# Performance work log

Hardware: AMD Instinct MI355X
Metric: run time of the kernel (lower is better)

Reference implementation:

```python
import jax, jax.numpy as jnp
import numpy as np

B, T, C, H = 4, 2048, 1024, 16
D = C // H


def setup_inputs() -> dict:
    key = jax.random.key(0)
    ks = jax.random.split(key, 5)
    s = C ** -0.5  # keep linear outputs O(1) like standard init
    x = jax.random.normal(ks[0], (B, T, C), dtype=jnp.float32)
    Wq = jax.random.normal(ks[1], (C, C), dtype=jnp.float32) * s
    Wk = jax.random.normal(ks[2], (C, C), dtype=jnp.float32) * s
    Wv = jax.random.normal(ks[3], (C, C), dtype=jnp.float32) * s
    Wproj = jax.random.normal(ks[4], (C, C), dtype=jnp.float32) * s
    alpha_raw = jnp.zeros((1, H, 1, 1), dtype=jnp.float32)
    beta_raw = jnp.zeros((1, H, 1, 1), dtype=jnp.float32)
    state = jnp.zeros((B, H, D, D), dtype=jnp.float32)
    return dict(x=x, Wq=Wq, Wk=Wk, Wv=Wv, Wproj=Wproj,
                alpha_raw=alpha_raw, beta_raw=beta_raw, state=state)


def reference(x, Wq, Wk, Wv, Wproj, alpha_raw, beta_raw, state):
    Bx, Tx, Cx = x.shape
    Hn = alpha_raw.shape[1]
    Dh = Cx // Hn
    # projections (torch Linear: x @ W^T), split heads -> (B, H, T, D)
    def proj(W):
        return (x @ W.T).reshape(Bx, Tx, Hn, Dh).transpose(0, 2, 1, 3)
    q, k, v = proj(Wq), proj(Wk), proj(Wv)
    # F.normalize(k, dim=-1) with eps=1e-12
    k = k / jnp.maximum(jnp.linalg.norm(k, axis=-1, keepdims=True), 1e-12)
    alpha = jax.nn.sigmoid(alpha_raw) * 0.5  # (1, H, 1, 1)
    beta = jax.nn.sigmoid(beta_raw) * 0.5

    def step(st, qkv):
        qt, kt, vt = qkv  # each (B, H, D)
        # y_t = q_t @ state^T
        y = jnp.einsum('bhe,bhde->bhd', qt, st)
        # Mk = state @ k_t
        Mk = jnp.einsum('bhde,bhe->bhd', st, kt)
        st = st - alpha * jnp.einsum('bhd,bhe->bhde', Mk, kt) \
                + beta * jnp.einsum('bhd,bhe->bhde', vt, kt)
        return st, y

    # scan over time: (T, B, H, D)
    qT = q.transpose(2, 0, 1, 3)
    kT = k.transpose(2, 0, 1, 3)
    vT = v.transpose(2, 0, 1, 3)
    state_f, ys = jax.lax.scan(step, state, (qT, kT, vT))
    y = ys.transpose(1, 0, 2, 3).reshape(Bx, Tx, Cx)  # (B, T, C)
    out = y @ Wproj.T
    return out, state_f
```

## Files before the change

kernel.cpp:

```cpp
#include <hip/hip_runtime.h>
#include <hip/hip_bf16.h>
#include <cstdint>

#define B_ 4
#define T_ 2048
#define C_ 1024
#define H_ 16
#define D_ 64
#define NC_ 32
#define L_ 64

typedef __attribute__((ext_vector_type(8))) short bf16x8;
typedef __attribute__((ext_vector_type(4))) float f32x4;

static __device__ __forceinline__ unsigned short f2bf(float f) {
  unsigned u = __float_as_uint(f);
  u += 0x7fff + ((u >> 16) & 1);
  return (unsigned short)(u >> 16);
}
static __device__ __forceinline__ float bf2f(unsigned short b) {
  return __uint_as_float(((unsigned)b) << 16);
}
static __device__ __forceinline__ int swz128(int row, int byte) {
  return row * 128 + (byte ^ ((row & 7) << 4));
}

#define LDS_BARRIER() asm volatile("s_waitcnt lgkmcnt(0)\ns_barrier" ::: "memory")

__global__ __launch_bounds__(256) void cvt_kernel(const float* __restrict__ src,
                                                  unsigned short* __restrict__ dst, int n) {
  int i = (blockIdx.x * 256 + threadIdx.x) * 4;
  if (i >= n) return;
  float4 v = *reinterpret_cast<const float4*>(src + i);
  ushort4 o;
  o.x = f2bf(v.x); o.y = f2bf(v.y); o.z = f2bf(v.z); o.w = f2bf(v.w);
  *reinterpret_cast<ushort4*>(dst + i) = o;
}

__global__ __launch_bounds__(256) void cvt_w_kernel(const float* __restrict__ wq,
                                                    const float* __restrict__ wk,
                                                    const float* __restrict__ wv,
                                                    const float* __restrict__ wp,
                                                    unsigned short* __restrict__ W3,
                                                    unsigned short* __restrict__ Wp) {
  const int g = blockIdx.x >> 10;
  const float* src = (g == 0) ? wq : (g == 1) ? wk : (g == 2) ? wv : wp;
  unsigned short* dst = (g < 3) ? (W3 + (long)g * 1048576) : Wp;
  int i = ((blockIdx.x & 1023) * 256 + threadIdx.x) * 4;
  float4 v = *reinterpret_cast<const float4*>(src + i);
  ushort4 o;
  o.x = f2bf(v.x); o.y = f2bf(v.y); o.z = f2bf(v.z); o.w = f2bf(v.w);
  *reinterpret_cast<ushort4*>(dst + i) = o;
}

template<int OUT_BF16>
__global__ __launch_bounds__(256) void gemm_bt(const unsigned short* __restrict__ A,
                                               const unsigned short* __restrict__ Bw,
                                               void* __restrict__ Cp,
                                               int M, int N, int K) {
  __shared__ __align__(16) unsigned short sA[128 * 32];
  __shared__ __align__(16) unsigned short sB[128 * 32];
  const int tid = threadIdx.x;
  const int wid = tid >> 6, lane = tid & 63;
  const int wm = wid >> 1, wn = wid & 1;
  const long blockM = (long)blockIdx.y * 128;
  const long blockN = (long)blockIdx.x * 128;

  f32x4 acc[4][4] = {};

  const int ar = lane >> 2;
  const int ac = (lane & 3) * 8;
  const unsigned short* Abase = A + (blockM + wid * 32 + ar) * (long)K + ac;
  const unsigned short* Bbase = Bw + (blockN + wid * 32 + ar) * (long)K + ac;
  char* sAb = (char*)sA + wid * 2048;
  char* sBb = (char*)sB + wid * 2048;

  for (int k0 = 0; k0 < K; k0 += 32) {
    __syncthreads();
    __builtin_amdgcn_global_load_lds((const __attribute__((address_space(1))) void*)(Abase + k0),
                                     (__attribute__((address_space(3))) void*)(sAb), 16, 0, 0);
    __builtin_amdgcn_global_load_lds((const __attribute__((address_space(1))) void*)(Abase + 16 * (long)K + k0),
                                     (__attribute__((address_space(3))) void*)(sAb + 1024), 16, 0, 0);
    __builtin_amdgcn_global_load_lds((const __attribute__((address_space(1))) void*)(Bbase + k0),
                                     (__attribute__((address_space(3))) void*)(sBb), 16, 0, 0);
    __builtin_amdgcn_global_load_lds((const __attribute__((address_space(1))) void*)(Bbase + 16 * (long)K + k0),
                                     (__attribute__((address_space(3))) void*)(sBb + 1024), 16, 0, 0);
    __syncthreads();

    const int koff = (lane >> 4) * 8;
    const int rA = wm * 64 + (lane & 15);
    const int rB = wn * 64 + (lane & 15);
    bf16x8 af[4], bfr[4];
#pragma unroll
    for (int m = 0; m < 4; ++m)
      af[m] = *reinterpret_cast<const bf16x8*>(&sA[(rA + m * 16) * 32 + koff]);
#pragma unroll
    for (int n = 0; n < 4; ++n)
      bfr[n] = *reinterpret_cast<const bf16x8*>(&sB[(rB + n * 16) * 32 + koff]);
#pragma unroll
    for (int m = 0; m < 4; ++m)
#pragma unroll
      for (int n = 0; n < 4; ++n)
        acc[m][n] = __builtin_amdgcn_mfma_f32_16x16x32_bf16(af[m], bfr[n], acc[m][n], 0, 0, 0);
  }

  const int cr = (lane >> 4) * 4;
  const int cc = lane & 15;
#pragma unroll
  for (int m = 0; m < 4; ++m) {
    long R = blockM + wm * 64 + m * 16 + cr;
#pragma unroll
    for (int n = 0; n < 4; ++n) {
      long Cc = blockN + wn * 64 + n * 16 + cc;
#pragma unroll
      for (int r = 0; r < 4; ++r) {
        if (OUT_BF16)
          ((unsigned short*)Cp)[(R + r) * (long)N + Cc] = f2bf(acc[m][n][r]);
        else
          ((float*)Cp)[(R + r) * (long)N + Cc] = acc[m][n][r];
      }
    }
  }
}

__global__ __launch_bounds__(256) void chunk_prep(
    unsigned short* __restrict__ qkv,
    const float* __restrict__ a_raw, const float* __restrict__ b_raw,
    unsigned short* __restrict__ Ubuf, unsigned short* __restrict__ Wbuf,
    unsigned short* __restrict__ SLbuf) {
  __shared__ __align__(16) unsigned short sK[64 * 64];
  __shared__ __align__(16) unsigned short sQ[64 * 64];
  __shared__ __align__(16) unsigned short sV[64 * 64];
  __shared__ float sA[64 * 64];

  const int blk = blockIdx.x;
  const int bh = blk >> 5, c = blk & 31;
  const int b = bh >> 4, h = bh & 15;
  const int tid = threadIdx.x;
  const int wid = tid >> 6, lane = tid & 63;

  const float alpha = 0.5f / (1.f + __expf(-a_raw[h]));
  const float beta  = 0.5f / (1.f + __expf(-b_raw[h]));

  {
    const int row = tid >> 2, cg = tid & 3;
    unsigned short* gp = qkv + (long)(b * 2048 + c * 64 + row) * 3072 + h * 64 + cg * 16;
    bf16x8 q0 = *(const bf16x8*)(gp);
    bf16x8 q1 = *(const bf16x8*)(gp + 8);
    bf16x8 k0 = *(const bf16x8*)(gp + 1024);
    bf16x8 k1 = *(const bf16x8*)(gp + 1024 + 8);
    bf16x8 v0 = *(const bf16x8*)(gp + 2048);
    bf16x8 v1 = *(const bf16x8*)(gp + 2048 + 8);
    float kf[16];
    float ss = 0.f;
#pragma unroll
    for (int i = 0; i < 8; ++i) { kf[i] = bf2f((unsigned short)k0[i]); ss += kf[i] * kf[i]; }
#pragma unroll
    for (int i = 0; i < 8; ++i) { kf[8 + i] = bf2f((unsigned short)k1[i]); ss += kf[8 + i] * kf[8 + i]; }
    ss += __shfl_xor(ss, 1);
    ss += __shfl_xor(ss, 2);
    const float inv = 1.f / fmaxf(sqrtf(ss), 1e-12f);
    bf16x8 n0, n1;
#pragma unroll
    for (int i = 0; i < 8; ++i) { n0[i] = (short)f2bf(kf[i] * inv); n1[i] = (short)f2bf(kf[8 + i] * inv); }
    *(bf16x8*)((char*)sK + swz128(row, cg * 32)) = n0;
    *(bf16x8*)((char*)sK + swz128(row, cg * 32 + 16)) = n1;
    *(bf16x8*)(gp + 1024) = n0;
    *(bf16x8*)(gp + 1024 + 8) = n1;
    *(bf16x8*)((char*)sQ + swz128(row, cg * 32)) = q0;
    *(bf16x8*)((char*)sQ + swz128(row, cg * 32 + 16)) = q1;
    *(bf16x8*)((char*)sV + row * 128 + cg * 32) = v0;
    *(bf16x8*)((char*)sV + row * 128 + cg * 32 + 16) = v1;
  }
  __syncthreads();

  const int rfrag = lane & 15, koff = (lane >> 4) * 8, crow = (lane >> 4) * 4;
  const int w2 = wid & 1;
  if (wid < 2) {
#pragma unroll
    for (int mt = 0; mt < 2; ++mt) {
      const int m = w2 * 2 + mt;
      const int ra = 16 * m + rfrag;
      f32x4 acc[4] = {};
#pragma unroll
      for (int ks = 0; ks < 2; ++ks) {
        bf16x8 af = *(const bf16x8*)((const char*)sK + swz128(ra, ks * 64 + koff * 2));
#pragma unroll
        for (int n = 0; n < 4; ++n) {
          bf16x8 bf = *(const bf16x8*)((const char*)sK + swz128(16 * n + rfrag, ks * 64 + koff * 2));
          acc[n] = __builtin_amdgcn_mfma_f32_16x16x32_bf16(af, bf, acc[n], 0, 0, 0);
        }
      }
#pragma unroll
      for (int n = 0; n < 4; ++n)
#pragma unroll
        for (int r = 0; r < 4; ++r)
          sA[(16 * m + crow + r) * 64 + 16 * n + rfrag] = acc[n][r];
    }
  } else {
#pragma unroll
    for (int mt = 0; mt < 2; ++mt) {
      const int m = w2 * 2 + mt;
      const int ra = 16 * m + rfrag;
      f32x4 acc[4] = {};
#pragma unroll
      for (int ks = 0; ks < 2; ++ks) {
        bf16x8 af = *(const bf16x8*)((const char*)sQ + swz128(ra, ks * 64 + koff * 2));
#pragma unroll
        for (int n = 0; n < 4; ++n) {
          bf16x8 bf = *(const bf16x8*)((const char*)sK + swz128(16 * n + rfrag, ks * 64 + koff * 2));
          acc[n] = __builtin_amdgcn_mfma_f32_16x16x32_bf16(af, bf, acc[n], 0, 0, 0);
        }
      }
#pragma unroll
      for (int n = 0; n < 4; ++n)
#pragma unroll
        for (int r = 0; r < 4; ++r) {
          int t = 16 * m + crow + r, j = 16 * n + rfrag;
          SLbuf[(long)blk * 4096 + t * 64 + j] = (j < t) ? f2bf(acc[n][r]) : (unsigned short)0;
        }
    }
  }
  __syncthreads();

  if (wid < 2) {
    const int d = lane;
    float x[64];
#pragma unroll
    for (int t = 0; t < 64; ++t) {
      float rhs;
      if (wid == 0) rhs = beta * bf2f(sV[t * 64 + d]);
      else          rhs = alpha * bf2f(*(const unsigned short*)((const char*)sK + swz128(t, 2 * d)));
      float s = 0.f;
#pragma unroll
      for (int j = 0; j < t; ++j) s = fmaf(sA[t * 64 + j], x[j], s);
      x[t] = rhs - alpha * s;
    }
    unsigned short* ob = (wid == 0 ? Ubuf : Wbuf) + (long)blk * 4096 + d;
#pragma unroll
    for (int t = 0; t < 64; ++t) ob[t * 64] = f2bf(x[t]);
  }
}

__global__ __launch_bounds__(256) void chunk_scan(
    const unsigned short* __restrict__ qkv,
    const unsigned short* __restrict__ Ubuf, const unsigned short* __restrict__ Wbuf,
    const unsigned short* __restrict__ SLbuf,
    const float* __restrict__ state_in, unsigned short* __restrict__ ybuf,
    float* __restrict__ state_out) {
  __shared__ __align__(16) unsigned short sQ[64 * 64];
  __shared__ __align__(16) unsigned short sW[64 * 64];
  __shared__ __align__(16) unsigned short sSL[64 * 64];
  __shared__ __align__(16) unsigned short sKT[64 * 64];
  __shared__ __align__(16) unsigned short sU[64 * 16];
  __shared__ __align__(16) unsigned short sGT[16 * 64];
  __shared__ __align__(16) unsigned short sS[16 * 64];

  const int blk = blockIdx.x;
  const int bh = blk >> 2, dq = blk & 3;
  const int b = bh >> 4, h = bh & 15;
  const int tid = threadIdx.x, wid = tid >> 6, lane = tid & 63;
  const int rfrag = lane & 15, koff = (lane >> 4) * 8, crow = (lane >> 4) * 4;
  const int row = tid >> 2, cg = tid & 3;

  const unsigned short* gpb = qkv + (long)(b * 2048 + row) * 3072 + h * 64 + cg * 16;
  const long tbb = ((long)(bh * 32) * 64 + row) * 64 + cg * 16;
  const long ubb = ((long)(bh * 32) * 64 + (tid >> 1)) * 64 + dq * 16 + (tid & 1) * 8;

  bf16x8 qv0, qv1, kv0, kv1, wv0, wv1, sl0, sl1, uv;
  {
    qv0 = *(const bf16x8*)gpb;
    qv1 = *(const bf16x8*)(gpb + 8);
    kv0 = *(const bf16x8*)(gpb + 1024);
    kv1 = *(const bf16x8*)(gpb + 1024 + 8);
    wv0 = *(const bf16x8*)(Wbuf + tbb);
    wv1 = *(const bf16x8*)(Wbuf + tbb + 8);
    sl0 = *(const bf16x8*)(SLbuf + tbb);
    sl1 = *(const bf16x8*)(SLbuf + tbb + 8);
    uv = (tid < 128) ? *(const bf16x8*)(Ubuf + ubb) : bf16x8{};
  }

  f32x4 sacc;
#pragma unroll
  for (int r = 0; r < 4; ++r)
    sacc[r] = state_in[(long)bh * 4096 + (dq * 16 + crow + r) * 64 + 16 * wid + rfrag];
#pragma unroll
  for (int r = 0; r < 4; ++r)
    *(unsigned short*)((char*)sS + swz128(crow + r, 2 * (16 * wid + rfrag))) = f2bf(sacc[r]);

  for (int c = 0; c < NC_; ++c) {
    *(bf16x8*)((char*)sQ + swz128(row, cg * 32)) = qv0;
    *(bf16x8*)((char*)sQ + swz128(row, cg * 32 + 16)) = qv1;
    *(bf16x8*)((char*)sW + swz128(row, cg * 32)) = wv0;
    *(bf16x8*)((char*)sW + swz128(row, cg * 32 + 16)) = wv1;
    *(bf16x8*)((char*)sSL + swz128(row, cg * 32)) = sl0;
    *(bf16x8*)((char*)sSL + swz128(row, cg * 32 + 16)) = sl1;
#pragma unroll
    for (int i = 0; i < 8; ++i) {
      *(unsigned short*)((char*)sKT + swz128(cg * 16 + i, 2 * row)) = (unsigned short)kv0[i];
      *(unsigned short*)((char*)sKT + swz128(cg * 16 + 8 + i, 2 * row)) = (unsigned short)kv1[i];
    }
    if (tid < 128) *(bf16x8*)((char*)sU + ((tid >> 1) * 16 + (tid & 1) * 8) * 2) = uv;

    {
      const int cn = (c + 1 < NC_) ? c + 1 : c;
      const unsigned short* gp = gpb + (long)cn * 64 * 3072;
      const long tb = tbb + (long)cn * 4096;
      qv0 = *(const bf16x8*)gp;
      qv1 = *(const bf16x8*)(gp + 8);
      kv0 = *(const bf16x8*)(gp + 1024);
      kv1 = *(const bf16x8*)(gp + 1024 + 8);
      wv0 = *(const bf16x8*)(Wbuf + tb);
      wv1 = *(const bf16x8*)(Wbuf + tb + 8);
      sl0 = *(const bf16x8*)(SLbuf + tb);
      sl1 = *(const bf16x8*)(SLbuf + tb + 8);
      if (tid < 128) uv = *(const bf16x8*)(Ubuf + ubb + (long)cn * 4096);
    }
    LDS_BARRIER();

    const int ta = 16 * wid + rfrag;
    f32x4 p = {};
    f32x4 yac = {};
#pragma unroll
    for (int ks = 0; ks < 2; ++ks) {
      bf16x8 afw = *(const bf16x8*)((const char*)sW + swz128(ta, ks * 64 + koff * 2));
      bf16x8 afq = *(const bf16x8*)((const char*)sQ + swz128(ta, ks * 64 + koff * 2));
      bf16x8 bS = *(const bf16x8*)((const char*)sS + swz128(rfrag, ks * 64 + koff * 2));
      p = __builtin_amdgcn_mfma_f32_16x16x32_bf16(afw, bS, p, 0, 0, 0);
      yac = __builtin_amdgcn_mfma_f32_16x16x32_bf16(afq, bS, yac, 0, 0, 0);
    }
#pragma unroll
    for (int r = 0; r < 4; ++r) {
      int t = 16 * wid + crow + r;
      float g = bf2f(sU[t * 16 + rfrag]) - p[r];
      *(unsigned short*)((char*)sGT + swz128(rfrag, 2 * t)) = f2bf(g);
    }
    LDS_BARRIER();

#pragma unroll
    for (int ks = 0; ks < 2; ++ks) {
      bf16x8 aSL = *(const bf16x8*)((const char*)sSL + swz128(ta, ks * 64 + koff * 2));
      bf16x8 bGT = *(const bf16x8*)((const char*)sGT + swz128(rfrag, ks * 64 + koff * 2));
      yac = __builtin_amdgcn_mfma_f32_16x16x32_bf16(aSL, bGT, yac, 0, 0, 0);
    }
#pragma unroll
    for (int r = 0; r < 4; ++r) {
      int t = 16 * wid + crow + r;
      ybuf[(long)(b * 2048 + c * 64 + t) * 1024 + h * 64 + dq * 16 + rfrag] = f2bf(yac[r]);
    }
#pragma unroll
    for (int ks = 0; ks < 2; ++ks) {
      bf16x8 aGT = *(const bf16x8*)((const char*)sGT + swz128(rfrag, ks * 64 + koff * 2));
      bf16x8 bKT = *(const bf16x8*)((const char*)sKT + swz128(16 * wid + rfrag, ks * 64 + koff * 2));
      sacc = __builtin_amdgcn_mfma_f32_16x16x32_bf16(aGT, bKT, sacc, 0, 0, 0);
    }
    LDS_BARRIER();

#pragma unroll
    for (int r = 0; r < 4; ++r)
      *(unsigned short*)((char*)sS + swz128(crow + r, 2 * (16 * wid + rfrag))) = f2bf(sacc[r]);
  }

#pragma unroll
  for (int r = 0; r < 4; ++r)
    state_out[(long)bh * 4096 + (dq * 16 + crow + r) * 64 + 16 * wid + rfrag] = sacc[r];
}

extern "C" void kernel_launch(void* const* d_in, const int* in_sizes, int n_in,
                              void* d_out, int out_size, void* d_ws, size_t ws_size,
                              hipStream_t stream) {
  (void)in_sizes; (void)n_in; (void)out_size; (void)ws_size;
  const float* x     = (const float*)d_in[0];
  const float* Wq    = (const float*)d_in[1];
  const float* Wk    = (const float*)d_in[2];
  const float* Wv    = (const float*)d_in[3];
  const float* Wproj = (const float*)d_in[4];
  const float* a_raw = (const float*)d_in[5];
  const float* b_raw = (const float*)d_in[6];
  const float* state = (const float*)d_in[7];

  char* ws = (char*)d_ws;
  unsigned short* xbf = (unsigned short*)ws;
  unsigned short* W3  = (unsigned short*)(ws + (16l << 20));
  unsigned short* Wp  = (unsigned short*)(ws + (22l << 20));
  unsigned short* qkv = (unsigned short*)(ws + (24l << 20));
  unsigned short* Ub  = (unsigned short*)(ws + (72l << 20));
  unsigned short* Wb  = (unsigned short*)(ws + (88l << 20));
  unsigned short* SLb = (unsigned short*)(ws + (104l << 20));
  float* out = (float*)d_out;
  float* state_out = out + (long)B_ * T_ * C_;

  cvt_kernel<<<dim3(8192), dim3(256), 0, stream>>>(x, xbf, 8388608);
  cvt_w_kernel<<<dim3(4096), dim3(256), 0, stream>>>(Wq, Wk, Wv, Wproj, W3, Wp);

  gemm_bt<1><<<dim3(3072 / 128, 8192 / 128), dim3(256), 0, stream>>>(xbf, W3, (void*)qkv, 8192, 3072, 1024);

  chunk_prep<<<dim3(2048), dim3(256), 0, stream>>>(qkv, a_raw, b_raw, Ub, Wb, SLb);
  chunk_scan<<<dim3(256), dim3(256), 0, stream>>>(qkv, Ub, Wb, SLb, state, xbf, state_out);

  gemm_bt<0><<<dim3(1024 / 128, 8192 / 128), dim3(256), 0, stream>>>(xbf, Wp, (void*)out, 8192, 1024, 1024);
}
```

Before: 211.5 us.

## Replace QKV projection GEMM with 256x256-tile pipelined direct-to-LDS kernel

Adds a new 512-thread GEMM kernel with 256x256 output tiles, double-buffered LDS staging via global_load_lds, swizzled LDS reads, and phase-interleaved prefetch with setprio around MFMA bursts. It replaces the 128x128 gemm_bt for the QKV projection to raise arithmetic intensity and overlap global loads with compute. It uses 128KB LDS per block, so occupancy is limited and the grid of 384 blocks may underfill or tail on the device. The output-projection GEMM remains on the old kernel.

```diff
diff --git a/kernel.cpp b/kernel.cpp
--- a/kernel.cpp
+++ b/kernel.cpp
@@ -53,6 +53,112 @@
   *reinterpret_cast<ushort4*>(dst + i) = o;
 }
 
+
+#define STAGE256(GP, GR0, KT, LOFF) do {                                          \
+    const unsigned short* _s = (GP) + ((GR0) + wid * 8 + lr8) * 1024L             \
+                               + (long)(KT) * 64 + skb * 8;                       \
+    char* _d = (char*)lds + (LOFF) + wid * 1024;                                  \
+    __builtin_amdgcn_global_load_lds((const __attribute__((address_space(1))) void*)_s,      \
+        (__attribute__((address_space(3))) void*)_d, 16, 0, 0);                   \
+    __builtin_amdgcn_global_load_lds((const __attribute__((address_space(1))) void*)(_s + 64 * 1024L), \
+        (__attribute__((address_space(3))) void*)(_d + 8192), 16, 0, 0);          \
+  } while (0)
+
+#define PHASE256(AO, BO, MH, NH, STG) do {                                        \
+    asm volatile("s_waitcnt vmcnt(6)" ::: "memory");                              \
+    bf16x8 av[4][2], bv[2][2];                                                    \
+    {                                                                             \
+      const char* ab = (const char*)lds + (AO) + (MH) * 16384 + arow;             \
+      const char* bb = (const char*)lds + (BO) + (NH) * 16384 + brow;             \
+      _Pragma("unroll")                                                           \
+      for (int j = 0; j < 4; ++j) {                                               \
+        av[j][0] = *(const bf16x8*)(ab + j * 4096 + cb0);                         \
+        av[j][1] = *(const bf16x8*)(ab + j * 4096 + cb1);                         \
+      }                                                                           \
+      _Pragma("unroll")                                                           \
+      for (int j2 = 0; j2 < 2; ++j2) {                                            \
+        bv[j2][0] = *(const bf16x8*)(bb + j2 * 8192 + cb0);                       \
+        bv[j2][1] = *(const bf16x8*)(bb + j2 * 8192 + cb1);                       \
+      }                                                                           \
+    }                                                                             \
+    STG;                                                                          \
+    __builtin_amdgcn_s_barrier();                                                 \
+    asm volatile("s_waitcnt lgkmcnt(0)" ::: "memory");                            \
+    __builtin_amdgcn_sched_barrier(0);                                            \
+    __builtin_amdgcn_s_setprio(1);                                                \
+    _Pragma("unroll")                                                             \
+    for (int j = 0; j < 4; ++j)                                                   \
+      _Pragma("unroll")                                                           \
+      for (int j2 = 0; j2 < 2; ++j2)                                              \
+        acc[(MH) * 4 + j][(NH) * 2 + j2] = __builtin_amdgcn_mfma_f32_16x16x32_bf16( \
+            av[j][0], bv[j2][0], acc[(MH) * 4 + j][(NH) * 2 + j2], 0, 0, 0);      \
+    _Pragma("unroll")                                                             \
+    for (int j = 0; j < 4; ++j)                                                   \
+      _Pragma("unroll")                                                           \
+      for (int j2 = 0; j2 < 2; ++j2)                                              \
+        acc[(MH) * 4 + j][(NH) * 2 + j2] = __builtin_amdgcn_mfma_f32_16x16x32_bf16( \
+            av[j][1], bv[j2][1], acc[(MH) * 4 + j][(NH) * 2 + j2], 0, 0, 0);      \
+    __builtin_amdgcn_s_setprio(0);                                                \
+    __builtin_amdgcn_s_barrier();                                                 \
+  } while (0)
+
+__global__ __launch_bounds__(512, 2) void gemm256_bt(
+    const unsigned short* __restrict__ A,
+    const unsigned short* __restrict__ Bw,
+    unsigned short* __restrict__ C, int N) {
+  __shared__ __align__(16) char lds[131072];
+  enum { EA = 0, EB = 32768, OA = 65536, OB = 98304, HF = 16384 };
+  const int tid = threadIdx.x;
+  const int wid = tid >> 6, lane = tid & 63;
+  const int wm = wid >> 2, wn = wid & 3;
+  const int f = lane & 15, g = lane >> 4;
+  const int lr8 = lane >> 3, lc = lane & 7;
+  const int skb = lc ^ lr8;
+  const long bM = (long)blockIdx.y * 256;
+  const long bN = (long)blockIdx.x * 256;
+  const int cb0 = ((0 + g) ^ (f & 7)) * 16;
+  const int cb1 = ((4 + g) ^ (f & 7)) * 16;
+  const int arow = (wm * 16 + f) * 128;
+  const int brow = (wn * 16 + f) * 128;
+
+  f32x4 acc[8][4] = {};
+
+  STAGE256(A, bM, 0, EA);
+  STAGE256(Bw, bN, 0, EB);
+  STAGE256(A, bM + 128, 0, EA + HF);
+  STAGE256(Bw, bN + 128, 0, EB + HF);
+  STAGE256(Bw, bN, 1, OB);
+  STAGE256(A, bM, 1, OA);
+  asm volatile("s_waitcnt vmcnt(8)" ::: "memory");
+  __builtin_amdgcn_s_barrier();
+
+  for (int i = 0; i < 8; ++i) {
+    const int todd = 2 * i + 1;
+    int te = 2 * i + 2; if (te > 14) te = 14;
+    int to = 2 * i + 3; if (to > 15) to = 15;
+    PHASE256(EA, EB, 0, 0, STAGE256(A, bM + 128, todd, OA + HF));
+    PHASE256(EA, EB, 1, 0, STAGE256(Bw, bN + 128, todd, OB + HF));
+    PHASE256(EA, EB, 0, 1, STAGE256(Bw, bN, te, EB));
+    PHASE256(EA, EB, 1, 1, STAGE256(A, bM, te, EA));
+    PHASE256(OA, OB, 0, 0, STAGE256(A, bM + 128, te, EA + HF));
+    PHASE256(OA, OB, 1, 0, STAGE256(Bw, bN + 128, te, EB + HF));
+    PHASE256(OA, OB, 0, 1, STAGE256(Bw, bN, to, OB));
+    PHASE256(OA, OB, 1, 1, STAGE256(A, bM, to, OA));
+  }
+
+#pragma unroll
+  for (int mf = 0; mf < 8; ++mf) {
+    long row = bM + (mf >> 2) * 128 + (mf & 3) * 32 + wm * 16 + g * 4;
+#pragma unroll
+    for (int nf = 0; nf < 4; ++nf) {
+      long col = bN + (nf >> 1) * 128 + (nf & 1) * 64 + wn * 16 + f;
+#pragma unroll
+      for (int r = 0; r < 4; ++r)
+        C[(row + r) * (long)N + col] = f2bf(acc[mf][nf][r]);
+    }
+  }
+}
+
 template<int OUT_BF16>
 __global__ __launch_bounds__(256) void gemm_bt(const unsigned short* __restrict__ A,
                                                const unsigned short* __restrict__ Bw,
@@ -332,8 +438,8 @@
 #pragma unroll
     for (int r = 0; r < 4; ++r) {
       int t = 16 * wid + crow + r;
-      float g = bf2f(sU[t * 16 + rfrag]) - p[r];
-      *(unsigned short*)((char*)sGT + swz128(rfrag, 2 * t)) = f2bf(g);
+      float gg = bf2f(sU[t * 16 + rfrag]) - p[r];
+      *(unsigned short*)((char*)sGT + swz128(rfrag, 2 * t)) = f2bf(gg);
     }
     LDS_BARRIER();
 
@@ -393,7 +499,7 @@
   cvt_kernel<<<dim3(8192), dim3(256), 0, stream>>>(x, xbf, 8388608);
   cvt_w_kernel<<<dim3(4096), dim3(256), 0, stream>>>(Wq, Wk, Wv, Wproj, W3, Wp);
 
-  gemm_bt<1><<<dim3(3072 / 128, 8192 / 128), dim3(256), 0, stream>>>(xbf, W3, (void*)qkv, 8192, 3072, 1024);
+  gemm256_bt<<<dim3(3072 / 256, 8192 / 256), dim3(512), 0, stream>>>(xbf, W3, qkv, 3072);
 
   chunk_prep<<<dim3(2048), dim3(256), 0, stream>>>(qkv, a_raw, b_raw, Ub, Wb, SLb);
   chunk_scan<<<dim3(256), dim3(256), 0, stream>>>(qkv, Ub, Wb, SLb, state, xbf, state_out);
```

Measured after the change: 209.5 us. Within noise of the previous version (-0.9%).
